# Optimization experiments

Hardware: AMD Instinct MI355X
Metric: run time of the kernel (lower is better)

## Reference

```python
import jax, jax.numpy as jnp
import numpy as np

N = 512    # nnodes
H = 8      # attention heads
C = 32     # gnn_repr_size (per head)
ER = 32    # edge_repr_size
FE = 3     # feat_emb_size
E = 16384  # edges (avg degree 32)


def gat_conv(x, edge_index, edge_attr, W, att_src, att_dst, We, att_edge, b):
    """PyG GATConv (edge_dim=1, concat=True, add_self_loops=True, eval mode)."""
    n = x.shape[0]
    h_, c_ = att_src.shape
    row, col = edge_index[0], edge_index[1]
    # self loops with fill_value='mean': mean of incoming edge_attr per target node
    deg = jax.ops.segment_sum(jnp.ones_like(edge_attr), col, num_segments=n)
    loop_attr = jax.ops.segment_sum(edge_attr, col, num_segments=n) / jnp.maximum(deg, 1.0)
    ar = jnp.arange(n)
    row = jnp.concatenate([row, ar])
    col = jnp.concatenate([col, ar])
    ea = jnp.concatenate([edge_attr, loop_attr])
    # node projections [n, H, C]
    h = (x @ W.T).reshape(n, h_, c_)
    a_src = jnp.sum(h * att_src, axis=-1)  # [n, H]
    a_dst = jnp.sum(h * att_dst, axis=-1)  # [n, H]
    e = (ea[:, None] @ We.T).reshape(-1, h_, c_)  # [E', H, C]
    a_e = jnp.sum(e * att_edge, axis=-1)          # [E', H]
    alpha = jax.nn.leaky_relu(a_src[row] + a_dst[col] + a_e, 0.2)
    # softmax over edges grouped by destination node
    amax = jax.ops.segment_max(alpha, col, num_segments=n)
    ex = jnp.exp(alpha - amax[col])
    denom = jax.ops.segment_sum(ex, col, num_segments=n)
    alpha = ex / (denom[col] + 1e-16)
    out = jax.ops.segment_sum(h[row] * alpha[..., None], col, num_segments=n)
    return out.reshape(n, h_ * c_) + b


def setup_inputs():
    key = jax.random.key(0)
    ks = jax.random.split(key, 24)
    s = 0.05
    HC = H * C
    in_len = N * ER + 3 * N + 3 * FE  # combiner1 input length
    return {
        "dist": jax.random.uniform(ks[0], (N, N), dtype=jnp.float32),
        "markov": jax.random.uniform(ks[1], (N, N), dtype=jnp.float32),
        "demand": jax.random.normal(ks[2], (N,), dtype=jnp.float32),
        "W_week": jax.random.normal(ks[3], (7, FE)) * s,
        "W_cap": jax.random.normal(ks[4], (26, FE)) * s,
        "W_veh": jax.random.normal(ks[5], (15, FE)) * s,
        "g1_W": jax.random.normal(ks[6], (HC, 1)) * s,
        "g1_att_src": jax.random.normal(ks[7], (H, C)) * s,
        "g1_att_dst": jax.random.normal(ks[8], (H, C)) * s,
        "g1_We": jax.random.normal(ks[9], (HC, 1)) * s,
        "g1_att_edge": jax.random.normal(ks[10], (H, C)) * s,
        "g1_b": jnp.zeros((HC,), dtype=jnp.float32),
        "g2_W": jax.random.normal(ks[11], (HC, HC)) * s,
        "g2_att_src": jax.random.normal(ks[12], (H, C)) * s,
        "g2_att_dst": jax.random.normal(ks[13], (H, C)) * s,
        "g2_We": jax.random.normal(ks[14], (HC, 1)) * s,
        "g2_att_edge": jax.random.normal(ks[15], (H, C)) * s,
        "g2_b": jnp.zeros((HC,), dtype=jnp.float32),
        "Wes": jax.random.normal(ks[16], (ER, 2 * HC)) * s,
        "bes": jnp.zeros((ER,), dtype=jnp.float32),
        "Wc1": jax.random.normal(ks[17], (N, in_len)) * 0.01,
        "bc1": jnp.zeros((N,), dtype=jnp.float32),
        "Wc2": jax.random.normal(ks[18], (N, N)) * s,
        "bc2": jnp.zeros((N,), dtype=jnp.float32),
        "stops": jax.random.randint(ks[19], (256,), 0, N),
        "edge_index": jax.random.randint(ks[20], (2, E), 0, N),
        "weekday": 3,
        "vehicles": 7,
        "capacity": 12,
    }


def reference(dist, markov, demand, W_week, W_cap, W_veh,
              g1_W, g1_att_src, g1_att_dst, g1_We, g1_att_edge, g1_b,
              g2_W, g2_att_src, g2_att_dst, g2_We, g2_att_edge, g2_b,
              Wes, bes, Wc1, bc1, Wc2, bc2,
              stops, edge_index, weekday, vehicles, capacity):
    n = dist.shape[0]
    dist = (dist - dist.min()) / (dist.max() - dist.min())
    x = demand[:, None]  # [n, 1]
    ea = markov[edge_index[0], edge_index[1]]  # [E]
    x = jax.nn.relu(gat_conv(x, edge_index, ea, g1_W, g1_att_src, g1_att_dst, g1_We, g1_att_edge, g1_b))
    x = jax.nn.relu(gat_conv(x, edge_index, ea, g2_W, g2_att_src, g2_att_dst, g2_We, g2_att_edge, g2_b))
    HC_ = x.shape[1]
    # all-pairs edge representation: concat(x[i], x[j]) over meshgrid -> [n*n, 2*HC]
    er = jnp.concatenate([
        jnp.broadcast_to(x[:, None, :], (n, n, HC_)),
        jnp.broadcast_to(x[None, :, :], (n, n, HC_)),
    ], axis=-1).reshape(n * n, 2 * HC_)
    er = (er @ Wes.T + bes).reshape(n, -1)  # [n, n*ER]
    week = jnp.broadcast_to(W_week[weekday], (n, W_week.shape[1]))
    cap = jnp.broadcast_to(W_cap[capacity], (n, W_cap.shape[1]))
    veh = jnp.broadcast_to(W_veh[vehicles], (n, W_veh.shape[1]))
    stop = jnp.broadcast_to(jnp.zeros((n,), dtype=dist.dtype).at[stops].set(1.0)[None, :], (n, n))
    feat = jnp.concatenate([er, dist, markov, week, cap, veh, stop], axis=1)
    out = jax.nn.relu(feat @ Wc1.T + bc1) @ Wc2.T + bc2
    return out
```

## Files before the change

### kernel.cpp

```cpp
#include <hip/hip_runtime.h>
#include <hip/hip_bf16.h>

typedef __hip_bfloat16 bf16;
typedef __attribute__((ext_vector_type(8))) short bf16x8;
typedef __attribute__((ext_vector_type(4))) float f32x4;

#define NNODE 512
#define NEDGE 16384
#define INLEN 17929
#define K1P   1088

#define WS_EA      0
#define WS_CSRC    16384
#define WS_CEA     32768
#define WS_DEG     49152
#define WS_STARTS  49664
#define WS_LATTR   50176
#define WS_MM      50688
#define WS_MMP     50690
#define WS_STOPV   50818
#define WS_AE      51330
#define WS_PS      51346
#define WS_H       55552
#define WS_G2WT    186624
#define WS_H2      317696
#define WS_ASRC    448768
#define WS_ADST    452864
#define WS_UV      456960
#define WS_K       489728
#define WS_APACK   490240
#define WS_BPACK   768768
#define WS_OUT1    1047296
#define WS_WC2B    1178368
#define WS_WESF    1309440
#define WS_ASRC2   1325824
#define WS_ADST2   1329920
#define WS_CURSOR  1334016
#define WS_DEGP    1334528
#define WS_LSUMP   1367296

static __device__ __forceinline__ unsigned short f2bfbits(float x){
  bf16 b = __float2bfloat16(x);
  union { bf16 b; unsigned short u; } c; c.b = b; return c.u;
}

__global__ __launch_bounds__(256)
void k_prep(const float* __restrict__ demand, const float* __restrict__ W1,
            const float* __restrict__ att_s, const float* __restrict__ att_d,
            const int* __restrict__ stops, const float* __restrict__ Wes,
            const float* __restrict__ dist, const float* __restrict__ markov,
            const int* __restrict__ eidx,
            const float* __restrict__ g1We, const float* __restrict__ g1ae,
            const float* __restrict__ g2We, const float* __restrict__ g2ae,
            const float* __restrict__ g2W,  const float* __restrict__ g2as,
            const float* __restrict__ g2ad, const float* __restrict__ Wc2,
            float* ws){
  int b = blockIdx.x, tid = threadIdx.x;
  if (b < 512){
    int hd = tid>>5, c = tid&31;
    float hv = demand[b] * W1[tid];
    ws[WS_H + b*256 + tid] = hv;
    float ps = hv * att_s[tid];
    float pd = hv * att_d[tid];
    for (int off=16; off; off>>=1){ ps += __shfl_down(ps,off,32); pd += __shfl_down(pd,off,32); }
    if (c==0){ ws[WS_ASRC + b*8+hd]=ps; ws[WS_ADST + b*8+hd]=pd; }
  } else if (b == 512){
    ws[WS_STOPV+tid] = 0.f; ws[WS_STOPV+256+tid] = 0.f;
    __syncthreads();
    ws[WS_STOPV + stops[tid]] = 1.0f;
    if (tid < 8){
      float s=0.f; for (int c=0;c<32;c++) s += g1We[tid*32+c]*g1ae[tid*32+c];
      ws[WS_AE+tid]=s;
    } else if (tid < 16){
      int h=tid-8; float s=0.f; for (int c=0;c<32;c++) s += g2We[h*32+c]*g2ae[h*32+c];
      ws[WS_AE+8+h]=s;
    }
  } else if (b < 515){
    for (int idx = (b-513)*8192 + tid; idx < (b-512)*8192; idx += 256){
      int k = idx>>8, c = idx&255;
      ws[WS_WESF+idx] = (k<32) ? Wes[k*512+c] : Wes[(k-32)*512+256+c];
    }
  } else if (b < 579){
    __shared__ float smn[256], smx[256];
    int p = b-515;
    float mn = 3.4e38f, mx = -3.4e38f;
    const float4* dv = (const float4*)(dist + p*4096);
    #pragma unroll
    for (int k=0;k<4;k++){
      float4 v = dv[k*256 + tid];
      mn = fminf(mn, fminf(fminf(v.x,v.y), fminf(v.z,v.w)));
      mx = fmaxf(mx, fmaxf(fmaxf(v.x,v.y), fmaxf(v.z,v.w)));
    }
    smn[tid]=mn; smx[tid]=mx; __syncthreads();
    for (int off=128; off; off>>=1){
      if (tid<off){ smn[tid]=fminf(smn[tid],smn[tid+off]); smx[tid]=fmaxf(smx[tid],smx[tid+off]); }
      __syncthreads();
    }
    if (tid==0){ ws[WS_MMP+p]=smn[0]; ws[WS_MMP+64+p]=smx[0]; }
  } else if (b < 643){
    __shared__ int   hd_[512];
    __shared__ float hf_[512];
    int k = b-579;
    hd_[tid]=0; hd_[256+tid]=0; hf_[tid]=0.f; hf_[256+tid]=0.f;
    __syncthreads();
    int e = k*256 + tid;
    int r = eidx[e], c = eidx[NEDGE+e];
    float a = markov[r*NNODE + c];
    ws[WS_EA+e] = a;
    atomicAdd(&hd_[c], 1);
    atomicAdd(&hf_[c], a);
    __syncthreads();
    ((int*)(ws+WS_DEGP))[k*512+tid]     = hd_[tid];
    ((int*)(ws+WS_DEGP))[k*512+256+tid] = hd_[256+tid];
    ws[WS_LSUMP + k*512+tid]     = hf_[tid];
    ws[WS_LSUMP + k*512+256+tid] = hf_[256+tid];
  } else if (b < 659){
    int j = b-643;
    const float* att = (j<8) ? g2as : g2ad;
    int h = j&7;
    float s = 0.f;
    for (int c=0;c<32;c++) s += att[h*32+c] * g2W[(h*32+c)*256 + tid];
    ws[WS_PS + j*256 + tid] = s;
  } else if (b < 675){
    __shared__ float T[64][65];
    int tb = b-659, tr = tb>>2, tc = tb&3;
    int w = tid>>6, c = tid&63;
    for (int k=0;k<16;k++){
      int r = k*4 + w;
      T[r][c] = g2W[(tr*64+r)*256 + tc*64 + c];
    }
    __syncthreads();
    for (int k=0;k<16;k++){
      int r = k*4 + w;
      ws[WS_G2WT + (tc*64+r)*256 + tr*64 + c] = T[c][r];
    }
  } else if (b == 675){
    ((int*)(ws+WS_CURSOR))[tid] = 0;
    ((int*)(ws+WS_CURSOR))[256+tid] = 0;
  } else {
    int blk = b - 676;
    const float4* src = (const float4*)(Wc2 + blk*4096);
    ushort4* dst = (ushort4*)((unsigned short*)(ws+WS_WC2B) + blk*4096);
    #pragma unroll
    for (int i=0;i<4;i++){
      float4 v = src[i*256+tid];
      ushort4 u;
      u.x = f2bfbits(v.x); u.y = f2bfbits(v.y);
      u.z = f2bfbits(v.z); u.w = f2bfbits(v.w);
      dst[i*256+tid] = u;
    }
  }
}

__global__ __launch_bounds__(512)
void k_scansc(const int* __restrict__ eidx, float* ws){
  __shared__ int sc[512];
  __shared__ int startS[512];
  __shared__ float rmn[64], rmx[64];
  int t = threadIdx.x, b = blockIdx.x;
  const int* dp = (const int*)(ws+WS_DEGP);
  int d = 0;
  for (int k=0;k<64;k++) d += dp[k*512+t];
  sc[t] = d; __syncthreads();
  for (int off=1; off<512; off<<=1){
    int v = (t>=off) ? sc[t-off] : 0; __syncthreads();
    sc[t] += v; __syncthreads();
  }
  startS[t] = sc[t]-d;
  if (b == 0){
    float l = 0.f;
    for (int k=0;k<64;k++) l += ws[WS_LSUMP+k*512+t];
    ((int*)(ws+WS_STARTS))[t] = startS[t];
    ((int*)(ws+WS_DEG))[t] = d;
    ws[WS_LATTR+t] = l / (float)(d>1 ? d : 1);
    if (t < 64){ rmn[t]=ws[WS_MMP+t]; rmx[t]=ws[WS_MMP+64+t]; }
    __syncthreads();
    if (t == 0){
      float mn=rmn[0], mx=rmx[0];
      for (int i=1;i<64;i++){ mn=fminf(mn,rmn[i]); mx=fmaxf(mx,rmx[i]); }
      ws[WS_MM]=mn; ws[WS_MM+1]=mx;
    }
  }
  __syncthreads();
  int e = b*512 + t;
  int c = eidx[NEDGE+e];
  int p = startS[c] + atomicAdd((int*)(ws+WS_CURSOR)+c, 1);
  ((int*)(ws+WS_CSRC))[p] = eidx[e];
  ws[WS_CEA+p] = ws[WS_EA+e];
}

template<int MODE>
__global__ __launch_bounds__(256)
void k_agg(const float* __restrict__ hbuf, const float* __restrict__ asrc,
           const float* __restrict__ adst, const int* __restrict__ csrc,
           const float* __restrict__ cea, const int* __restrict__ starts,
           const int* __restrict__ deg, const float* __restrict__ lattr,
           const float* __restrict__ AEp, const float* __restrict__ bvec,
           const float* __restrict__ dist, const float* __restrict__ markov,
           float* ws){
  int t = blockIdx.x, tid = threadIdx.x, hd = tid>>5;
  __shared__ int   srcE[256];
  __shared__ float eaE[256];
  __shared__ float Lall[256*8];
  __shared__ float AE[8], mh[8], dh[8], sw[8];
  __shared__ float xrow[256], uvrow[64];
  if (tid<8) AE[tid]=AEp[tid];
  __syncthreads();
  int d = deg[t], s0 = starts[t];
  if (d > 256) d = 256;
  for (int e=tid; e<d; e+=256){ srcE[e]=csrc[s0+e]; eaE[e]=cea[s0+e]; }
  __syncthreads();
  {
    int h8 = tid&7;
    float adt = adst[t*8+h8], aeh = AE[h8];
    for (int e = tid>>3; e < d; e += 32){
      float a = asrc[srcE[e]*8+h8] + adt + eaE[e]*aeh;
      Lall[e*8+h8] = a>=0.f ? a : 0.2f*a;
    }
  }
  __syncthreads();
  {
    int h = tid>>5, j = tid&31;
    float aself = asrc[t*8+h] + adst[t*8+h] + lattr[t]*AE[h];
    aself = aself>=0.f ? aself : 0.2f*aself;
    float mm = aself;
    for (int e=j; e<d; e+=32) mm = fmaxf(mm, Lall[e*8+h]);
    for (int off=16; off; off>>=1) mm = fmaxf(mm, __shfl_down(mm,off,32));
    mm = __shfl(mm, 0, 32);
    float dd = 0.f;
    for (int e=j; e<d; e+=32) dd += __expf(Lall[e*8+h]-mm);
    for (int off=16; off; off>>=1) dd += __shfl_down(dd,off,32);
    if (j==0){
      float se = __expf(aself-mm);
      mh[h]=mm; dh[h]=dd+se+1e-16f; sw[h]=se;
    }
  }
  __syncthreads();
  {
    int h8 = tid&7;
    for (int e = tid>>3; e < d; e += 32)
      Lall[e*8+h8] = __expf(Lall[e*8+h8] - mh[h8]);
  }
  __syncthreads();
  float a0 = sw[hd]*hbuf[t*256+tid], a1=0.f, a2=0.f, a3=0.f;
  int e = 0;
  for (; e+4<=d; e+=4){
    a0 += Lall[(e+0)*8+hd]*hbuf[srcE[e+0]*256+tid];
    a1 += Lall[(e+1)*8+hd]*hbuf[srcE[e+1]*256+tid];
    a2 += Lall[(e+2)*8+hd]*hbuf[srcE[e+2]*256+tid];
    a3 += Lall[(e+3)*8+hd]*hbuf[srcE[e+3]*256+tid];
  }
  for (; e<d; e++) a0 += Lall[e*8+hd]*hbuf[srcE[e]*256+tid];
  float v = fmaxf(((a0+a1)+(a2+a3))/dh[hd] + bvec[tid], 0.f);
  xrow[tid] = v;
  __syncthreads();
  if (MODE == 1){
    const float* g2wt = ws + WS_G2WT;
    float h0=0.f,h1=0.f,h2=0.f,h3=0.f;
    for (int c=0;c<256;c+=4){
      h0 += xrow[c+0]*g2wt[(c+0)*256+tid];
      h1 += xrow[c+1]*g2wt[(c+1)*256+tid];
      h2 += xrow[c+2]*g2wt[(c+2)*256+tid];
      h3 += xrow[c+3]*g2wt[(c+3)*256+tid];
    }
    ws[WS_H2 + t*256 + tid] = (h0+h1)+(h2+h3);
    if (tid < 64){
      int j = tid>>2, q = tid&3;
      const float* pr = ws + WS_PS + j*256 + q*64;
      const float* xr = xrow + q*64;
      float p = 0.f;
      for (int c=0;c<64;c++) p += xr[c]*pr[c];
      p += __shfl_down(p,2,4);
      p += __shfl_down(p,1,4);
      if (q==0){
        if (j<8) ws[WS_ASRC2 + t*8+j] = p;
        else     ws[WS_ADST2 + t*8+(j-8)] = p;
      }
    }
  } else {
    int k = tid>>2, q = tid&3;
    const float* wr = ws + WS_WESF + k*256 + q*64;
    const float* xr = xrow + q*64;
    float p = 0.f;
    for (int c=0;c<64;c++) p += xr[c]*wr[c];
    p += __shfl_down(p,2,4);
    p += __shfl_down(p,1,4);
    if (q==0){ ws[WS_UV + t*64+k] = p; uvrow[k] = p; }
    __syncthreads();
    float mn = ws[WS_MM], mx = ws[WS_MM+1];
    float inv = 1.0f/(mx-mn);
    bf16* ap = (bf16*)(ws+WS_APACK);
    const float* mrow = markov + t*512;
    for (int j=tid; j<K1P; j+=256){
      float v2;
      if (j<32)        v2 = uvrow[j];
      else if (j<544)  v2 = (dist[t*512 + j-32] - mn) * inv;
      else if (j<1056) v2 = mrow[j-544];
      else             v2 = 0.f;
      ap[(size_t)t*K1P + j] = __float2bfloat16(v2);
    }
  }
}

__global__ __launch_bounds__(1024)
void k_skpack(const float* __restrict__ Wc1, const float* __restrict__ bc1,
              const float* __restrict__ bes, const float* __restrict__ Wweek,
              const float* __restrict__ Wcap, const float* __restrict__ Wveh,
              const int* __restrict__ wd, const int* __restrict__ vh,
              const int* __restrict__ cp, float* ws){
  int o = blockIdx.x, tid = threadIdx.x;
  __shared__ float besf[32];
  __shared__ float red[512];
  __shared__ float red2[16];
  if (tid<32) besf[tid] = bes[tid];
  __syncthreads();
  const float* wr = Wc1 + (size_t)o*INLEN;
  bf16* bp  = (bf16*)(ws+WS_BPACK);
  float be = besf[tid&31];
  const float* uvp = ws + WS_UV + ((tid>>5)<<6) + 32 + (tid&31);
  float sP = 0.f, tP0=0.f, tP1=0.f, tP2=0.f, tP3=0.f;
  #pragma unroll
  for (int i=0;i<16;i+=4){
    float w0 = wr[tid + 1024*(i+0)];
    float w1 = wr[tid + 1024*(i+1)];
    float w2 = wr[tid + 1024*(i+2)];
    float w3 = wr[tid + 1024*(i+3)];
    float u0 = uvp[2048*(i+0)];
    float u1 = uvp[2048*(i+1)];
    float u2 = uvp[2048*(i+2)];
    float u3 = uvp[2048*(i+3)];
    sP += (w0+w1)+(w2+w3);
    tP0 += w0*(u0+be);
    tP1 += w1*(u1+be);
    tP2 += w2*(u2+be);
    tP3 += w3*(u3+be);
  }
  float tP = (tP0+tP1)+(tP2+tP3);
  if (tid < 512) tP += ws[WS_STOPV+tid] * wr[17417+tid];
  if (tid < 9){
    int g = tid/3, f = tid-g*3;
    float sv = (g==0) ? Wweek[wd[0]*3+f]
             : (g==1) ? Wcap[cp[0]*3+f]
                      : Wveh[vh[0]*3+f];
    tP += sv * wr[17408+tid];
  }
  int lane = tid&63, w = tid>>6;
  sP += __shfl_down(sP, 32, 64);
  if (lane < 32) red[w*32 + lane] = sP;
  for (int off=32; off; off>>=1) tP += __shfl_down(tP, off, 64);
  if (lane == 0) red2[w] = tP;
  __syncthreads();
  if (tid < 32){
    float s = 0.f;
    #pragma unroll
    for (int k=0;k<16;k++) s += red[k*32+tid];
    bp[(size_t)o*K1P + tid] = __float2bfloat16(s);
    bp[(size_t)o*K1P + 1056 + tid] = __float2bfloat16(0.f);
  } else if (tid == 32){
    float s = 0.f;
    #pragma unroll
    for (int k=0;k<16;k++) s += red2[k];
    ws[WS_K+o] = s + bc1[o];
  }
  bp[(size_t)o*K1P + 32 + tid] = __float2bfloat16(wr[16384+tid]);
}

template<bool RELU, bool BF16OUT>
__global__ __launch_bounds__(512)
void gemm_mfma(const bf16* __restrict__ A, const bf16* __restrict__ B,
               const float* __restrict__ bias, float* __restrict__ Cf,
               bf16* __restrict__ Cb, int M, int N, int K){
  __shared__ short Als[2][4096];
  __shared__ short Bls[2][4096];
  const int tid = threadIdx.x;
  const int bm = blockIdx.y*64, bn = blockIdx.x*64;
  const int wave = tid>>6, lane = tid&63;
  const int wm = wave>>2, wn = wave&3;
  const int r = lane&15, q = lane>>4;
  f32x4 acc[2] = {};
  const int lrow = tid>>3, lk8 = tid&7;
  const bf16* Ag = A + (size_t)(bm+lrow)*K + lk8*8;
  const bf16* Bg = B + (size_t)(bn+lrow)*K + lk8*8;
  const int sidx = ((lk8>>2)*256 + (lk8&3)*64 + lrow)*8;
  const int nk = K>>6;
  float4 av = *(const float4*)(Ag);
  float4 bv = *(const float4*)(Bg);
  *(float4*)(&Als[0][sidx]) = av;
  *(float4*)(&Bls[0][sidx]) = bv;
  __syncthreads();
  for (int kk=0; kk<nk; kk++){
    int cur = kk&1, nxt = cur^1;
    if (kk+1 < nk){
      av = *(const float4*)(Ag + (kk+1)*64);
      bv = *(const float4*)(Bg + (kk+1)*64);
    }
    #pragma unroll
    for (int kk2=0; kk2<2; kk2++){
      bf16x8 bfr = *(const bf16x8*)(&Bls[cur][(kk2*256 + q*64 + wn*16 + r)*8]);
      #pragma unroll
      for (int i=0;i<2;i++){
        bf16x8 af = *(const bf16x8*)(&Als[cur][(kk2*256 + q*64 + wm*32 + i*16 + r)*8]);
        acc[i] = __builtin_amdgcn_mfma_f32_16x16x32_bf16(af, bfr, acc[i], 0,0,0);
      }
    }
    if (kk+1 < nk){
      __syncthreads();
      *(float4*)(&Als[nxt][sidx]) = av;
      *(float4*)(&Bls[nxt][sidx]) = bv;
      __syncthreads();
    }
  }
  #pragma unroll
  for (int i=0;i<2;i++){
    int row = bm + wm*32 + i*16 + q*4;
    int col = bn + wn*16 + r;
    float bi = bias ? bias[col] : 0.f;
    #pragma unroll
    for (int g=0; g<4; g++){
      float v = acc[i][g] + bi;
      if (RELU) v = fmaxf(v, 0.f);
      if (BF16OUT) Cb[(size_t)(row+g)*N + col] = __float2bfloat16(v);
      else         Cf[(size_t)(row+g)*N + col] = v;
    }
  }
}

extern "C" void kernel_launch(void* const* d_in, const int* in_sizes, int n_in,
                              void* d_out, int out_size, void* d_ws, size_t ws_size,
                              hipStream_t stream){
  const float* dist   = (const float*)d_in[0];
  const float* markov = (const float*)d_in[1];
  const float* demand = (const float*)d_in[2];
  const float* Wweek  = (const float*)d_in[3];
  const float* Wcap   = (const float*)d_in[4];
  const float* Wveh   = (const float*)d_in[5];
  const float* g1W    = (const float*)d_in[6];
  const float* g1as   = (const float*)d_in[7];
  const float* g1ad   = (const float*)d_in[8];
  const float* g1We   = (const float*)d_in[9];
  const float* g1ae   = (const float*)d_in[10];
  const float* g1b    = (const float*)d_in[11];
  const float* g2W    = (const float*)d_in[12];
  const float* g2as   = (const float*)d_in[13];
  const float* g2ad   = (const float*)d_in[14];
  const float* g2We   = (const float*)d_in[15];
  const float* g2ae   = (const float*)d_in[16];
  const float* g2b    = (const float*)d_in[17];
  const float* Wes    = (const float*)d_in[18];
  const float* bes    = (const float*)d_in[19];
  const float* Wc1    = (const float*)d_in[20];
  const float* bc1    = (const float*)d_in[21];
  const float* Wc2    = (const float*)d_in[22];
  const float* bc2    = (const float*)d_in[23];
  const int*   stops  = (const int*)d_in[24];
  const int*   eidx   = (const int*)d_in[25];
  const int*   wd     = (const int*)d_in[26];
  const int*   vh     = (const int*)d_in[27];
  const int*   cp     = (const int*)d_in[28];
  float* out = (float*)d_out;
  float* ws = (float*)d_ws;

  const int*   csrc   = (const int*)(ws+WS_CSRC);
  const float* cea    = ws+WS_CEA;
  const int*   starts = (const int*)(ws+WS_STARTS);
  const int*   deg    = (const int*)(ws+WS_DEG);
  const float* lattr  = ws+WS_LATTR;

  k_prep<<<740,256,0,stream>>>(demand, g1W, g1as, g1ad, stops, Wes, dist, markov, eidx,
                               g1We, g1ae, g2We, g2ae, g2W, g2as, g2ad, Wc2, ws);
  k_scansc<<<32,512,0,stream>>>(eidx, ws);
  k_agg<1><<<512,256,0,stream>>>(ws+WS_H, ws+WS_ASRC, ws+WS_ADST, csrc, cea, starts, deg,
                                 lattr, ws+WS_AE, g1b, dist, markov, ws);
  k_agg<2><<<512,256,0,stream>>>(ws+WS_H2, ws+WS_ASRC2, ws+WS_ADST2, csrc, cea, starts, deg,
                                 lattr, ws+WS_AE+8, g2b, dist, markov, ws);
  k_skpack<<<512,1024,0,stream>>>(Wc1, bc1, bes, Wweek, Wcap, Wveh, wd, vh, cp, ws);
  gemm_mfma<true,true><<<dim3(8,8),512,0,stream>>>((const bf16*)(ws+WS_APACK), (const bf16*)(ws+WS_BPACK),
                                                   ws+WS_K, nullptr, (bf16*)(ws+WS_OUT1), 512, 512, K1P);
  gemm_mfma<false,false><<<dim3(8,8),512,0,stream>>>((const bf16*)(ws+WS_OUT1), (const bf16*)(ws+WS_WC2B),
                                                     bc2, out, nullptr, 512, 512, 512);
}
```

Baseline: 204.4 us.

## Split-K both MFMA GEMMs with atomic accumulation and widen aggregation unroll

Both final GEMMs, which previously launched only 64 blocks, now use split-K over a z grid dimension (4 for the first, 2 for the second) so more CUs are busy. Partial results go into fp32 buffers with atomicAdd, and those buffers are zeroed by extra blocks added to the prep kernel. The bias, ReLU and bf16 conversion of the first GEMM move into a new small epilogue kernel. The edge-aggregation inner loop is also unrolled to 8 independent accumulators for more memory-level parallelism, at the cost of atomic traffic, an extra launch and a nondeterministic summation order.

```diff
diff --git a/kernel.cpp b/kernel.cpp
--- a/kernel.cpp
+++ b/kernel.cpp
@@ -38,6 +38,7 @@
 #define WS_CURSOR  1334016
 #define WS_DEGP    1334528
 #define WS_LSUMP   1367296
+#define WS_OUT1F   1400064
 
 static __device__ __forceinline__ unsigned short f2bfbits(float x){
   bf16 b = __float2bfloat16(x);
@@ -54,7 +55,7 @@
             const float* __restrict__ g2We, const float* __restrict__ g2ae,
             const float* __restrict__ g2W,  const float* __restrict__ g2as,
             const float* __restrict__ g2ad, const float* __restrict__ Wc2,
-            float* ws){
+            float* __restrict__ outp, float* ws){
   int b = blockIdx.x, tid = threadIdx.x;
   if (b < 512){
     int hd = tid>>5, c = tid&31;
@@ -137,7 +138,7 @@
   } else if (b == 675){
     ((int*)(ws+WS_CURSOR))[tid] = 0;
     ((int*)(ws+WS_CURSOR))[256+tid] = 0;
-  } else {
+  } else if (b < 740){
     int blk = b - 676;
     const float4* src = (const float4*)(Wc2 + blk*4096);
     ushort4* dst = (ushort4*)((unsigned short*)(ws+WS_WC2B) + blk*4096);
@@ -149,6 +150,15 @@
       u.z = f2bfbits(v.z); u.w = f2bfbits(v.w);
       dst[i*256+tid] = u;
     }
+  } else {
+    int blk = b - 740;
+    float4 z = {0.f,0.f,0.f,0.f};
+    float4* o1f = (float4*)(ws + WS_OUT1F);
+    float4* op  = (float4*)outp;
+    o1f[blk*512 + tid] = z;
+    o1f[blk*512 + 256 + tid] = z;
+    op[blk*512 + tid] = z;
+    op[blk*512 + 256 + tid] = z;
   }
 }
 
@@ -242,16 +252,20 @@
       Lall[e*8+h8] = __expf(Lall[e*8+h8] - mh[h8]);
   }
   __syncthreads();
-  float a0 = sw[hd]*hbuf[t*256+tid], a1=0.f, a2=0.f, a3=0.f;
+  float a0 = sw[hd]*hbuf[t*256+tid], a1=0.f, a2=0.f, a3=0.f, a4=0.f, a5=0.f, a6=0.f, a7=0.f;
   int e = 0;
-  for (; e+4<=d; e+=4){
+  for (; e+8<=d; e+=8){
     a0 += Lall[(e+0)*8+hd]*hbuf[srcE[e+0]*256+tid];
     a1 += Lall[(e+1)*8+hd]*hbuf[srcE[e+1]*256+tid];
     a2 += Lall[(e+2)*8+hd]*hbuf[srcE[e+2]*256+tid];
     a3 += Lall[(e+3)*8+hd]*hbuf[srcE[e+3]*256+tid];
+    a4 += Lall[(e+4)*8+hd]*hbuf[srcE[e+4]*256+tid];
+    a5 += Lall[(e+5)*8+hd]*hbuf[srcE[e+5]*256+tid];
+    a6 += Lall[(e+6)*8+hd]*hbuf[srcE[e+6]*256+tid];
+    a7 += Lall[(e+7)*8+hd]*hbuf[srcE[e+7]*256+tid];
   }
   for (; e<d; e++) a0 += Lall[e*8+hd]*hbuf[srcE[e]*256+tid];
-  float v = fmaxf(((a0+a1)+(a2+a3))/dh[hd] + bvec[tid], 0.f);
+  float v = fmaxf((((a0+a1)+(a2+a3))+((a4+a5)+(a6+a7)))/dh[hd] + bvec[tid], 0.f);
   xrow[tid] = v;
   __syncthreads();
   if (MODE == 1){
@@ -365,64 +379,82 @@
   bp[(size_t)o*K1P + 32 + tid] = __float2bfloat16(wr[16384+tid]);
 }
 
-template<bool RELU, bool BF16OUT>
+template<bool ADDB>
 __global__ __launch_bounds__(512)
-void gemm_mfma(const bf16* __restrict__ A, const bf16* __restrict__ B,
-               const float* __restrict__ bias, float* __restrict__ Cf,
-               bf16* __restrict__ Cb, int M, int N, int K){
+void gemm_split(const bf16* __restrict__ A, const bf16* __restrict__ B,
+                const float* __restrict__ bias, float* __restrict__ C,
+                int N, int K){
   __shared__ short Als[2][4096];
   __shared__ short Bls[2][4096];
   const int tid = threadIdx.x;
   const int bm = blockIdx.y*64, bn = blockIdx.x*64;
+  const int kz = blockIdx.z, NS = gridDim.z;
+  const int nkT = K>>6;
+  const int kb = (nkT*kz)/NS, ke = (nkT*(kz+1))/NS, cnt = ke-kb;
   const int wave = tid>>6, lane = tid&63;
   const int wm = wave>>2, wn = wave&3;
   const int r = lane&15, q = lane>>4;
   f32x4 acc[2] = {};
   const int lrow = tid>>3, lk8 = tid&7;
-  const bf16* Ag = A + (size_t)(bm+lrow)*K + lk8*8;
-  const bf16* Bg = B + (size_t)(bn+lrow)*K + lk8*8;
+  const bf16* Ag = A + (size_t)(bm+lrow)*K + kb*64 + lk8*8;
+  const bf16* Bg = B + (size_t)(bn+lrow)*K + kb*64 + lk8*8;
   const int sidx = ((lk8>>2)*256 + (lk8&3)*64 + lrow)*8;
-  const int nk = K>>6;
   float4 av = *(const float4*)(Ag);
   float4 bv = *(const float4*)(Bg);
   *(float4*)(&Als[0][sidx]) = av;
   *(float4*)(&Bls[0][sidx]) = bv;
   __syncthreads();
-  for (int kk=0; kk<nk; kk++){
+  for (int kk=0; kk<cnt; kk++){
     int cur = kk&1, nxt = cur^1;
-    if (kk+1 < nk){
+    if (kk+1 < cnt){
       av = *(const float4*)(Ag + (kk+1)*64);
       bv = *(const float4*)(Bg + (kk+1)*64);
     }
     #pragma unroll
-    for (int kk2=0; kk2<2; kk2++){
-      bf16x8 bfr = *(const bf16x8*)(&Bls[cur][(kk2*256 + q*64 + wn*16 + r)*8]);
+    for (int k2=0; k2<2; k2++){
+      bf16x8 bfr = *(const bf16x8*)(&Bls[cur][(k2*256 + q*64 + wn*16 + r)*8]);
       #pragma unroll
       for (int i=0;i<2;i++){
-        bf16x8 af = *(const bf16x8*)(&Als[cur][(kk2*256 + q*64 + wm*32 + i*16 + r)*8]);
+        bf16x8 af = *(const bf16x8*)(&Als[cur][(k2*256 + q*64 + wm*32 + i*16 + r)*8]);
         acc[i] = __builtin_amdgcn_mfma_f32_16x16x32_bf16(af, bfr, acc[i], 0,0,0);
       }
     }
-    if (kk+1 < nk){
+    if (kk+1 < cnt){
       __syncthreads();
       *(float4*)(&Als[nxt][sidx]) = av;
       *(float4*)(&Bls[nxt][sidx]) = bv;
       __syncthreads();
     }
   }
+  const int col = bn + wn*16 + r;
+  const float bi = (ADDB && kz==0) ? bias[col] : 0.f;
   #pragma unroll
   for (int i=0;i<2;i++){
     int row = bm + wm*32 + i*16 + q*4;
-    int col = bn + wn*16 + r;
-    float bi = bias ? bias[col] : 0.f;
     #pragma unroll
-    for (int g=0; g<4; g++){
-      float v = acc[i][g] + bi;
-      if (RELU) v = fmaxf(v, 0.f);
-      if (BF16OUT) Cb[(size_t)(row+g)*N + col] = __float2bfloat16(v);
-      else         Cf[(size_t)(row+g)*N + col] = v;
-    }
-  }
+    for (int g=0; g<4; g++)
+      atomicAdd(&C[(size_t)(row+g)*N + col], acc[i][g] + bi);
+  }
+}
+
+__global__ __launch_bounds__(256)
+void k_ep1(float* ws){
+  int idx = (blockIdx.x*256 + threadIdx.x)*8;
+  const float4* s  = (const float4*)(ws + WS_OUT1F + idx);
+  const float4* kv = (const float4*)(ws + WS_K + (idx&511));
+  float4 v0 = s[0], v1 = s[1];
+  float4 k0 = kv[0], k1 = kv[1];
+  ushort4 u0, u1;
+  u0.x = f2bfbits(fmaxf(v0.x+k0.x, 0.f));
+  u0.y = f2bfbits(fmaxf(v0.y+k0.y, 0.f));
+  u0.z = f2bfbits(fmaxf(v0.z+k0.z, 0.f));
+  u0.w = f2bfbits(fmaxf(v0.w+k0.w, 0.f));
+  u1.x = f2bfbits(fmaxf(v1.x+k1.x, 0.f));
+  u1.y = f2bfbits(fmaxf(v1.y+k1.y, 0.f));
+  u1.z = f2bfbits(fmaxf(v1.z+k1.z, 0.f));
+  u1.w = f2bfbits(fmaxf(v1.w+k1.w, 0.f));
+  ushort4* d = (ushort4*)((unsigned short*)(ws+WS_OUT1) + idx);
+  d[0] = u0; d[1] = u1;
 }
 
 extern "C" void kernel_launch(void* const* d_in, const int* in_sizes, int n_in,
@@ -466,16 +498,17 @@
   const int*   deg    = (const int*)(ws+WS_DEG);
   const float* lattr  = ws+WS_LATTR;
 
-  k_prep<<<740,256,0,stream>>>(demand, g1W, g1as, g1ad, stops, Wes, dist, markov, eidx,
-                               g1We, g1ae, g2We, g2ae, g2W, g2as, g2ad, Wc2, ws);
+  k_prep<<<868,256,0,stream>>>(demand, g1W, g1as, g1ad, stops, Wes, dist, markov, eidx,
+                               g1We, g1ae, g2We, g2ae, g2W, g2as, g2ad, Wc2, out, ws);
   k_scansc<<<32,512,0,stream>>>(eidx, ws);
   k_agg<1><<<512,256,0,stream>>>(ws+WS_H, ws+WS_ASRC, ws+WS_ADST, csrc, cea, starts, deg,
                                  lattr, ws+WS_AE, g1b, dist, markov, ws);
   k_agg<2><<<512,256,0,stream>>>(ws+WS_H2, ws+WS_ASRC2, ws+WS_ADST2, csrc, cea, starts, deg,
                                  lattr, ws+WS_AE+8, g2b, dist, markov, ws);
   k_skpack<<<512,1024,0,stream>>>(Wc1, bc1, bes, Wweek, Wcap, Wveh, wd, vh, cp, ws);
-  gemm_mfma<true,true><<<dim3(8,8),512,0,stream>>>((const bf16*)(ws+WS_APACK), (const bf16*)(ws+WS_BPACK),
-                                                   ws+WS_K, nullptr, (bf16*)(ws+WS_OUT1), 512, 512, K1P);
-  gemm_mfma<false,false><<<dim3(8,8),512,0,stream>>>((const bf16*)(ws+WS_OUT1), (const bf16*)(ws+WS_WC2B),
-                                                     bc2, out, nullptr, 512, 512, 512);
-}
+  gemm_split<false><<<dim3(8,8,4),512,0,stream>>>((const bf16*)(ws+WS_APACK), (const bf16*)(ws+WS_BPACK),
+                                                  nullptr, ws+WS_OUT1F, 512, K1P);
+  k_ep1<<<128,256,0,stream>>>(ws);
+  gemm_split<true><<<dim3(8,8,2),512,0,stream>>>((const bf16*)(ws+WS_OUT1), (const bf16*)(ws+WS_WC2B),
+                                                 bc2, out, 512, 512);
+}
```

Measured after the change: 193.1 us. -5.5%, faster.
